# Kernel tuning notes

Measured on AMD Instinct MI355X. Metric: run time of the kernel, lower is better.

Reference implementation:

```python
import jax, jax.numpy as jnp
import numpy as np

N_NODES = 100000
N_FEAT = 512
HIDDEN = 64
N_CLASSES = 40
N_EDGES = 3200000
K = 10
ALPHA = 0.1


def setup_inputs() -> dict:
    key = jax.random.key(0)
    k1, k2, k3, k4 = jax.random.split(key, 4)
    x = jax.random.normal(k1, (N_NODES, N_FEAT), dtype=jnp.float32)
    # Glorot-ish scaled linear weights
    W1 = jax.random.normal(k2, (N_FEAT, HIDDEN), dtype=jnp.float32) / np.sqrt(N_FEAT)
    b1 = jnp.zeros((HIDDEN,), dtype=jnp.float32)
    W2 = jax.random.normal(k3, (HIDDEN, N_CLASSES), dtype=jnp.float32) / np.sqrt(HIDDEN)
    b2 = jnp.zeros((N_CLASSES,), dtype=jnp.float32)
    edge_index = jax.random.randint(k4, (2, N_EDGES), 0, N_NODES, dtype=jnp.int64)
    return {"x": x, "W1": W1, "b1": b1, "W2": W2, "b2": b2, "edge_index": edge_index}


def reference(x, W1, b1, W2, b2, edge_index):
    n = x.shape[0]
    # MLP (dropout is identity in eval mode)
    h = jnp.maximum(x @ W1 + b1, 0.0)
    h = h @ W2 + b2  # [N, C]

    # gcn_norm with self-loops: A_hat = D^{-1/2} (A + I) D^{-1/2}
    loops = jnp.arange(n, dtype=edge_index.dtype)
    row = jnp.concatenate([edge_index[0], loops])  # source (gather)
    col = jnp.concatenate([edge_index[1], loops])  # target (scatter)
    deg = jax.ops.segment_sum(jnp.ones(row.shape, dtype=h.dtype), col, num_segments=n)
    dinv = jnp.where(deg > 0, jax.lax.rsqrt(deg), 0.0)
    norm = dinv[row] * dinv[col]  # [E + N]

    h0 = h

    def step(z, _):
        msg = norm[:, None] * z[row]                      # gather + scale
        agg = jax.ops.segment_sum(msg, col, num_segments=n)  # scatter-add
        z = ALPHA * h0 + (1.0 - ALPHA) * agg
        return z, None

    z, _ = jax.lax.scan(step, h0, None, length=K)
    return jax.nn.log_softmax(z, axis=1)
```

## Files before the change

kernel.cpp:

```cpp
#include <hip/hip_runtime.h>
#include <hip/hip_bf16.h>
#include <hip/hip_fp16.h>

#define N_NODES   100000
#define N_FEAT    512
#define HIDDEN    64
#define N_CLASSES 40
#define KITER     10
#define ALPHA     0.1f
#define ZP        64
#define HPITCH    72

typedef __attribute__((ext_vector_type(8))) short bf16x8;
typedef __attribute__((ext_vector_type(4))) float f32x4;

__device__ __forceinline__ float bf2f(unsigned short u) {
    union { unsigned int i; float f; } c;
    c.i = ((unsigned int)u) << 16;
    return c.f;
}
__device__ __forceinline__ unsigned short f2bf(float f) {
    union { float f; unsigned int u; } c; c.f = f;
    unsigned int r = c.u + 0x7FFFu + ((c.u >> 16) & 1u);
    return (unsigned short)(r >> 16);
}

__global__ void zero_flags_kernel(int* __restrict__ flags) {
    if (threadIdx.x < 2) flags[threadIdx.x] = 0;
}

__global__ void detect_float_kernel(const unsigned short* __restrict__ w1raw,
                                    int* __restrict__ flags) {
    int i = blockIdx.x * blockDim.x + threadIdx.x;
    if (i < 32768) {
        unsigned short u = w1raw[i];
        if ((u & 0x7F80u) == 0x7F80u) atomicAdd(&flags[0], 1);
    }
}

__global__ void detect_edge_kernel(const int* __restrict__ ei, int* __restrict__ flags) {
    int i = blockIdx.x * blockDim.x + threadIdx.x;
    if (i < 2048) {
        if (ei[2 * i + 1] != 0) atomicAdd(&flags[1], 1);
    }
}

__device__ __forceinline__ int edge_row(const int* ei, int e, int E, int i64f) {
    return i64f ? ei[2 * e] : ei[e];
}
__device__ __forceinline__ int edge_col(const int* ei, int e, int E, int i64f) {
    return i64f ? ei[2 * E + 2 * e] : ei[E + e];
}

__global__ void pack_w1_kernel(const void* __restrict__ W1p, const int* __restrict__ flags,
                               unsigned short* __restrict__ pb) {
    int idx = blockIdx.x * 256 + threadIdx.x;
    int j    = idx & 7;
    int lane = (idx >> 3) & 63;
    int ktnt = idx >> 9;
    int kt = ktnt & 15, nt = ktnt >> 4;
    int k = kt * 32 + (lane >> 4) * 8 + j;
    int n = nt * 16 + (lane & 15);
    unsigned short v;
    if (flags[0] > 0) v = f2bf(((const float*)W1p)[k * HIDDEN + n]);
    else              v = ((const unsigned short*)W1p)[k * HIDDEN + n];
    pb[idx] = v;
}

__global__ void pack_w2_kernel(const void* __restrict__ W2p, const int* __restrict__ flags,
                               unsigned short* __restrict__ pb2) {
    int idx = blockIdx.x * 256 + threadIdx.x;
    if (idx >= 3072) return;
    int j    = idx & 7;
    int lane = (idx >> 3) & 63;
    int ktnt = idx >> 9;
    int kt = ktnt & 1, nt = ktnt >> 1;
    int k = kt * 32 + (lane >> 4) * 8 + j;
    int n = nt * 16 + (lane & 15);
    unsigned short v = 0;
    if (n < N_CLASSES) {
        if (flags[0] > 0) v = f2bf(((const float*)W2p)[k * N_CLASSES + n]);
        else              v = ((const unsigned short*)W2p)[k * N_CLASSES + n];
    }
    pb2[idx] = v;
}

__global__ __launch_bounds__(256) void mlp_kernel(
    const void* __restrict__ xp,
    const unsigned short* __restrict__ pb,
    const unsigned short* __restrict__ pb2,
    const void* __restrict__ b1p,
    const void* __restrict__ b2p,
    const int* __restrict__ flags,
    float* __restrict__ h0,
    __half* __restrict__ zh0)
{
    __shared__ unsigned short hsb[16 * HPITCH];
    const int t    = threadIdx.x;
    const int wave = t >> 6;
    const int lane = t & 63;
    const int quad = lane >> 4;
    const int ml   = lane & 15;
    const int base = blockIdx.x * 16;
    const int isf32 = flags[0] > 0;

    const bf16x8* pbv = (const bf16x8*)pb;

    f32x4 acc = {0.f, 0.f, 0.f, 0.f};
    if (!isf32) {
        const unsigned short* xrow = (const unsigned short*)xp
                                   + (size_t)(base + ml) * N_FEAT + quad * 8;
        #pragma unroll
        for (int kt = 0; kt < 16; ++kt) {
            bf16x8 a = *(const bf16x8*)(xrow + kt * 32);
            bf16x8 b = pbv[(wave * 16 + kt) * 64 + lane];
            acc = __builtin_amdgcn_mfma_f32_16x16x32_bf16(a, b, acc, 0, 0, 0);
        }
    } else {
        const float* xf = (const float*)xp + (size_t)(base + ml) * N_FEAT + quad * 8;
        #pragma unroll
        for (int kt = 0; kt < 16; ++kt) {
            float4 lo = *(const float4*)(xf + kt * 32);
            float4 hi = *(const float4*)(xf + kt * 32 + 4);
            bf16x8 a;
            a[0] = (short)f2bf(lo.x); a[1] = (short)f2bf(lo.y);
            a[2] = (short)f2bf(lo.z); a[3] = (short)f2bf(lo.w);
            a[4] = (short)f2bf(hi.x); a[5] = (short)f2bf(hi.y);
            a[6] = (short)f2bf(hi.z); a[7] = (short)f2bf(hi.w);
            bf16x8 b = pbv[(wave * 16 + kt) * 64 + lane];
            acc = __builtin_amdgcn_mfma_f32_16x16x32_bf16(a, b, acc, 0, 0, 0);
        }
    }

    float b1v = isf32 ? ((const float*)b1p)[wave * 16 + ml]
                      : bf2f(((const unsigned short*)b1p)[wave * 16 + ml]);
    #pragma unroll
    for (int r = 0; r < 4; ++r)
        hsb[(quad * 4 + r) * HPITCH + wave * 16 + ml] = f2bf(fmaxf(acc[r] + b1v, 0.0f));
    __syncthreads();

    if (wave < 3) {
        const bf16x8* pb2v = (const bf16x8*)pb2;
        f32x4 acc2 = {0.f, 0.f, 0.f, 0.f};
        #pragma unroll
        for (int kt = 0; kt < 2; ++kt) {
            bf16x8 a = *(const bf16x8*)(hsb + ml * HPITCH + kt * 32 + quad * 8);
            bf16x8 b = pb2v[(wave * 2 + kt) * 64 + lane];
            acc2 = __builtin_amdgcn_mfma_f32_16x16x32_bf16(a, b, acc2, 0, 0, 0);
        }
        int n = wave * 16 + ml;
        if (n < N_CLASSES) {
            float b2v = isf32 ? ((const float*)b2p)[n] : bf2f(((const unsigned short*)b2p)[n]);
            #pragma unroll
            for (int r = 0; r < 4; ++r) {
                int node = base + quad * 4 + r;
                float v = acc2[r] + b2v;
                h0[(size_t)node * N_CLASSES + n] = v;
                zh0[(size_t)node * ZP + n] = __float2half(v);
            }
        }
    }
}

__global__ void zero_cnt_kernel(int* __restrict__ cnt) {
    int i = blockIdx.x * blockDim.x + threadIdx.x;
    if (i < N_NODES) cnt[i] = 0;
}

__global__ void count_kernel(const int* __restrict__ ei, const int* __restrict__ flags,
                             int* __restrict__ cnt, int E) {
    int e = blockIdx.x * blockDim.x + threadIdx.x;
    int i64f = flags[1] == 0;
    if (e < E) atomicAdd(&cnt[edge_col(ei, e, E, i64f)], 1);
}

__global__ void dinv_kernel(const int* __restrict__ cnt, float* __restrict__ dinv) {
    int i = blockIdx.x * blockDim.x + threadIdx.x;
    if (i < N_NODES) dinv[i] = rsqrtf((float)cnt[i] + 1.0f);
}

__global__ __launch_bounds__(1024) void scan_kernel(
    const int* __restrict__ cnt, int* __restrict__ rptr, int* __restrict__ wpos, int E)
{
    __shared__ int wsum[16];
    __shared__ int carry_s, tiletot_s;
    const int t = threadIdx.x, wave = t >> 6, lane = t & 63;
    if (t == 0) carry_s = 0;
    __syncthreads();
    for (int base = 0; base < N_NODES; base += 4096) {
        int i0 = base + t * 4;
        int v0 = (i0 + 0 < N_NODES) ? cnt[i0 + 0] : 0;
        int v1 = (i0 + 1 < N_NODES) ? cnt[i0 + 1] : 0;
        int v2 = (i0 + 2 < N_NODES) ? cnt[i0 + 2] : 0;
        int v3 = (i0 + 3 < N_NODES) ? cnt[i0 + 3] : 0;
        int tl = v0 + v1 + v2 + v3;
        int sc = tl;
        #pragma unroll
        for (int off = 1; off < 64; off <<= 1) {
            int u = __shfl_up(sc, off, 64);
            if (lane >= off) sc += u;
        }
        if (lane == 63) wsum[wave] = sc;
        int wexcl = sc - tl;
        __syncthreads();
        if (wave == 0) {
            int wv = (lane < 16) ? wsum[lane] : 0;
            int ws = wv;
            #pragma unroll
            for (int off = 1; off < 16; off <<= 1) {
                int u = __shfl_up(ws, off, 64);
                if (lane >= off) ws += u;
            }
            if (lane < 16) wsum[lane] = ws - wv;
            if (lane == 15) tiletot_s = ws;
        }
        __syncthreads();
        int P  = carry_s + wsum[wave] + wexcl;
        int e0 = P, e1 = P + v0, e2 = e1 + v1, e3 = e2 + v2;
        if (i0 + 0 < N_NODES) { rptr[i0 + 0] = e0; wpos[i0 + 0] = e0; }
        if (i0 + 1 < N_NODES) { rptr[i0 + 1] = e1; wpos[i0 + 1] = e1; }
        if (i0 + 2 < N_NODES) { rptr[i0 + 2] = e2; wpos[i0 + 2] = e2; }
        if (i0 + 3 < N_NODES) { rptr[i0 + 3] = e3; wpos[i0 + 3] = e3; }
        __syncthreads();
        if (t == 0) carry_s += tiletot_s;
        __syncthreads();
    }
    if (t == 0) rptr[N_NODES] = E;
}

__global__ void fill_kernel(const int* __restrict__ ei, const int* __restrict__ flags,
                            const float* __restrict__ dinv, int* __restrict__ wpos,
                            int2* __restrict__ srn, int E)
{
    int e = blockIdx.x * blockDim.x + threadIdx.x;
    int i64f = flags[1] == 0;
    if (e < E) {
        int r = edge_row(ei, e, E, i64f);
        int c = edge_col(ei, e, E, i64f);
        int pos = atomicAdd(&wpos[c], 1);
        srn[pos] = make_int2(r, __float_as_int(dinv[r] * dinv[c]));
    }
}

__global__ __launch_bounds__(256) void prop_kernel(
    const __half* __restrict__ zh, const float* __restrict__ h0,
    const float* __restrict__ dinv, const int* __restrict__ rptr,
    const int2* __restrict__ srn, __half* __restrict__ zout, int E)
{
    const int wave = threadIdx.x >> 6;
    const int lane = threadIdx.x & 63;
    const int g    = lane >> 4;
    const int l    = lane & 15;
    const int node = blockIdx.x * 16 + wave * 4 + g;
    const int c0   = l * 4;

    const int beg = rptr[node];
    const int end = rptr[node + 1];
    int nch = (end - beg + 15) >> 4;
    int m1    = max(nch, __shfl_xor(nch, 16, 64));
    int maxch = max(m1,  __shfl_xor(m1, 32, 64));

    float di = dinv[node];
    uint2 zzs = *(const uint2*)(zh + ((size_t)node << 6) + c0);
    float h00 = 0.f, h01 = 0.f, h02 = 0.f, h03 = 0.f;
    if (c0 < N_CLASSES) {
        const float* hp = h0 + (size_t)node * N_CLASSES + c0;
        h00 = hp[0]; h01 = hp[1]; h02 = hp[2]; h03 = hp[3];
    }

    float a0 = 0.f, a1 = 0.f, a2 = 0.f, a3 = 0.f;
    float b0 = 0.f, b1 = 0.f, b2 = 0.f, b3 = 0.f;

    for (int ch = 0; ch < maxch; ++ch) {
        int idx  = beg + ch * 16 + l;
        bool v   = idx < end;
        int cidx = v ? idx : beg;
        cidx = min(cidx, E - 1);
        int2 ew  = srn[cidx];
        int   sw = ew.x;
        float nw = v ? __int_as_float(ew.y) : 0.0f;

        #pragma unroll
        for (int i = 0; i < 16; i += 2) {
            int   s0 = __shfl(sw, (g << 4) + i,     64);
            float n0 = __shfl(nw, (g << 4) + i,     64);
            int   s1 = __shfl(sw, (g << 4) + i + 1, 64);
            float n1 = __shfl(nw, (g << 4) + i + 1, 64);
            uint2 z0 = *(const uint2*)(zh + ((size_t)s0 << 6) + c0);
            uint2 z1 = *(const uint2*)(zh + ((size_t)s1 << 6) + c0);
            const __half2* p0 = (const __half2*)&z0;
            const __half2* p1 = (const __half2*)&z1;
            float2 f00 = __half22float2(p0[0]);
            float2 f01 = __half22float2(p0[1]);
            float2 f10 = __half22float2(p1[0]);
            float2 f11 = __half22float2(p1[1]);
            a0 = fmaf(n0, f00.x, a0); a1 = fmaf(n0, f00.y, a1);
            a2 = fmaf(n0, f01.x, a2); a3 = fmaf(n0, f01.y, a3);
            b0 = fmaf(n1, f10.x, b0); b1 = fmaf(n1, f10.y, b1);
            b2 = fmaf(n1, f11.x, b2); b3 = fmaf(n1, f11.y, b3);
        }
    }

    if (c0 < N_CLASSES) {
        const __half2* ps = (const __half2*)&zzs;
        float2 s01 = __half22float2(ps[0]);
        float2 s23 = __half22float2(ps[1]);
        float dd = di * di;
        float o0 = ALPHA * h00 + (1.0f - ALPHA) * (a0 + b0 + dd * s01.x);
        float o1 = ALPHA * h01 + (1.0f - ALPHA) * (a1 + b1 + dd * s01.y);
        float o2 = ALPHA * h02 + (1.0f - ALPHA) * (a2 + b2 + dd * s23.x);
        float o3 = ALPHA * h03 + (1.0f - ALPHA) * (a3 + b3 + dd * s23.y);
        __half2 q01 = __floats2half2_rn(o0, o1);
        __half2 q23 = __floats2half2_rn(o2, o3);
        uint2 st;
        st.x = *(unsigned int*)&q01;
        st.y = *(unsigned int*)&q23;
        *(uint2*)(zout + ((size_t)node << 6) + c0) = st;
    }
}

__global__ __launch_bounds__(256) void lsm_kernel(
    const __half* __restrict__ zh, const int* __restrict__ flags, void* __restrict__ outp)
{
    const int wave = threadIdx.x >> 6;
    const int lane = threadIdx.x & 63;
    const int node = blockIdx.x * 4 + wave;
    const int isf32 = flags[0] > 0;

    float v = (lane < N_CLASSES) ? __half2float(zh[(size_t)node * ZP + lane]) : -1e30f;
    float m = v;
    #pragma unroll
    for (int o = 32; o; o >>= 1) m = fmaxf(m, __shfl_xor(m, o, 64));
    float e = (lane < N_CLASSES) ? expf(v - m) : 0.0f;
    float s = e;
    #pragma unroll
    for (int o = 32; o; o >>= 1) s += __shfl_xor(s, o, 64);
    float ls = logf(s);
    if (lane < N_CLASSES) {
        float r = v - m - ls;
        size_t idx = (size_t)node * N_CLASSES + lane;
        if (isf32) ((float*)outp)[idx] = r;
        else       ((__hip_bfloat16*)outp)[idx] = __float2bfloat16(r);
    }
}

extern "C" void kernel_launch(void* const* d_in, const int* in_sizes, int n_in,
                              void* d_out, int out_size, void* d_ws, size_t ws_size,
                              hipStream_t stream)
{
    const void* x  = d_in[0];
    const void* W1 = d_in[1];
    const void* b1 = d_in[2];
    const void* W2 = d_in[3];
    const void* b2 = d_in[4];
    const int* ei = (const int*)d_in[5];
    const int E = in_sizes[5] / 2;

    char* ws = (char*)d_ws;
    size_t off = 0;
    auto carve = [&](size_t bytes) -> void* {
        void* p = ws + off;
        off = (off + bytes + 255) & ~(size_t)255;
        return p;
    };
    float*  h0    = (float*) carve((size_t)N_NODES * N_CLASSES * 4);
    __half* zhA   = (__half*)carve((size_t)N_NODES * ZP * 2);
    __half* zhB   = (__half*)carve((size_t)N_NODES * ZP * 2);
    int*    cnt   = (int*)   carve((size_t)N_NODES * 4);
    float*  dinv  = (float*) carve((size_t)N_NODES * 4);
    int*    rptr  = (int*)   carve((size_t)(N_NODES + 1) * 4);
    int*    wpos  = (int*)   carve((size_t)N_NODES * 4);
    int2*   srn   = (int2*)  carve((size_t)E * 8);
    unsigned short* pb  = (unsigned short*)carve(32768 * 2);
    unsigned short* pb2 = (unsigned short*)carve(3072 * 2);
    int*    flags = (int*)   carve(2 * sizeof(int));
    (void)ws_size; (void)n_in; (void)out_size;

    const int nodeBlocks = N_NODES / 4;
    const int mlpBlocks  = N_NODES / 16;
    const int propBlocks = N_NODES / 16;
    const int nThreads1  = (N_NODES + 255) / 256;
    const int eBlocks    = (E + 255) / 256;

    zero_flags_kernel<<<1, 64, 0, stream>>>(flags);
    detect_float_kernel<<<128, 256, 0, stream>>>((const unsigned short*)W1, flags);
    detect_edge_kernel<<<8, 256, 0, stream>>>(ei, flags);
    pack_w1_kernel<<<128, 256, 0, stream>>>(W1, flags, pb);
    pack_w2_kernel<<<12, 256, 0, stream>>>(W2, flags, pb2);

    mlp_kernel<<<mlpBlocks, 256, 0, stream>>>(x, pb, pb2, b1, b2, flags, h0, zhA);

    zero_cnt_kernel<<<nThreads1, 256, 0, stream>>>(cnt);
    count_kernel<<<eBlocks, 256, 0, stream>>>(ei, flags, cnt, E);
    dinv_kernel<<<nThreads1, 256, 0, stream>>>(cnt, dinv);
    scan_kernel<<<1, 1024, 0, stream>>>(cnt, rptr, wpos, E);
    fill_kernel<<<eBlocks, 256, 0, stream>>>(ei, flags, dinv, wpos, srn, E);

    const __half* zin = zhA;
    __half* zout = zhB;
    const __half* zlast = zhA;
    for (int it = 0; it < KITER; ++it) {
        prop_kernel<<<propBlocks, 256, 0, stream>>>(zin, h0, dinv, rptr, srn, zout, E);
        zlast = zout;
        zin = zout;
        zout = (zout == zhB) ? zhA : zhB;
    }

    lsm_kernel<<<nodeBlocks, 256, 0, stream>>>(zlast, flags, d_out);
}
```

Before: 1.274 ms.

## Store dinv-prescaled features and drop per-edge weights; window CSR fill by destination

Propagation state is now stored as dinv-scaled features, so each edge needs only a source index and the per-edge normalization weight disappears. This halves the CSR edge payload and removes a multiply per gathered element. A dummy zero row at index N_NODES replaces per-lane validity masking. The CSR fill kernel now makes eight windowed passes over destination ranges to localize its atomics and scattered writes, at the cost of re-reading edges. Scaling by dinv before fp16 storage, then dividing back in log-softmax, changes rounding behaviour.

New measurement: 1.300 ms. 2.1% more time.

```diff
diff --git a/kernel.cpp b/kernel.cpp
--- a/kernel.cpp
+++ b/kernel.cpp
@@ -10,6 +10,10 @@
 #define ALPHA     0.1f
 #define ZP        64
 #define HPITCH    72
+#define NPASS     8
+#define WIN       (N_NODES / NPASS)
+#define FILLB     2048
+#define SLOTS     7
 
 typedef __attribute__((ext_vector_type(8))) short bf16x8;
 typedef __attribute__((ext_vector_type(4))) float f32x4;
@@ -92,6 +96,7 @@
     const void* __restrict__ b1p,
     const void* __restrict__ b2p,
     const int* __restrict__ flags,
+    const float* __restrict__ dinv,
     float* __restrict__ h0,
     __half* __restrict__ zh0)
 {
@@ -156,7 +161,7 @@
                 int node = base + quad * 4 + r;
                 float v = acc2[r] + b2v;
                 h0[(size_t)node * N_CLASSES + n] = v;
-                zh0[(size_t)node * ZP + n] = __float2half(v);
+                zh0[(size_t)node * ZP + n] = __float2half(v * dinv[node]);
             }
         }
     }
@@ -177,6 +182,12 @@
 __global__ void dinv_kernel(const int* __restrict__ cnt, float* __restrict__ dinv) {
     int i = blockIdx.x * blockDim.x + threadIdx.x;
     if (i < N_NODES) dinv[i] = rsqrtf((float)cnt[i] + 1.0f);
+}
+
+__global__ void zero_pad_kernel(__half* __restrict__ a, __half* __restrict__ b) {
+    int t = threadIdx.x;
+    if (t < ZP)            a[(size_t)N_NODES * ZP + t]        = __float2half(0.0f);
+    else if (t < 2 * ZP)   b[(size_t)N_NODES * ZP + (t - ZP)] = __float2half(0.0f);
 }
 
 __global__ __launch_bounds__(1024) void scan_kernel(
@@ -228,24 +239,44 @@
     if (t == 0) rptr[N_NODES] = E;
 }
 
-__global__ void fill_kernel(const int* __restrict__ ei, const int* __restrict__ flags,
-                            const float* __restrict__ dinv, int* __restrict__ wpos,
-                            int2* __restrict__ srn, int E)
-{
-    int e = blockIdx.x * blockDim.x + threadIdx.x;
-    int i64f = flags[1] == 0;
-    if (e < E) {
-        int r = edge_row(ei, e, E, i64f);
-        int c = edge_col(ei, e, E, i64f);
-        int pos = atomicAdd(&wpos[c], 1);
-        srn[pos] = make_int2(r, __float_as_int(dinv[r] * dinv[c]));
+__global__ __launch_bounds__(256) void fill8_kernel(
+    const int* __restrict__ ei, const int* __restrict__ flags,
+    int* __restrict__ wpos, int* __restrict__ srcidx, int E)
+{
+    const int i64f = flags[1] == 0;
+    const int t0 = blockIdx.x * 256 + threadIdx.x;
+    const int stride = FILLB * 256;
+    int rk[SLOTS], ck[SLOTS];
+    #pragma unroll
+    for (int k = 0; k < SLOTS; ++k) {
+        int e = t0 + k * stride;
+        rk[k] = -1; ck[k] = -1;
+        if (e < E) { rk[k] = edge_row(ei, e, E, i64f); ck[k] = edge_col(ei, e, E, i64f); }
+    }
+    #pragma unroll
+    for (int p = 0; p < NPASS; ++p) {
+        int lo = p * WIN;
+        #pragma unroll
+        for (int k = 0; k < SLOTS; ++k) {
+            if ((unsigned)(ck[k] - lo) < (unsigned)WIN) {
+                int pos = atomicAdd(&wpos[ck[k]], 1);
+                srcidx[pos] = rk[k];
+            }
+        }
+        for (int e = t0 + SLOTS * stride; e < E; e += stride) {
+            int c = edge_col(ei, e, E, i64f);
+            if ((unsigned)(c - lo) < (unsigned)WIN) {
+                int pos = atomicAdd(&wpos[c], 1);
+                srcidx[pos] = edge_row(ei, e, E, i64f);
+            }
+        }
     }
 }
 
 __global__ __launch_bounds__(256) void prop_kernel(
     const __half* __restrict__ zh, const float* __restrict__ h0,
     const float* __restrict__ dinv, const int* __restrict__ rptr,
-    const int2* __restrict__ srn, __half* __restrict__ zout, int E)
+    const int* __restrict__ srcidx, __half* __restrict__ zout)
 {
     const int wave = threadIdx.x >> 6;
     const int lane = threadIdx.x & 63;
@@ -261,7 +292,7 @@
     int maxch = max(m1,  __shfl_xor(m1, 32, 64));
 
     float di = dinv[node];
-    uint2 zzs = *(const uint2*)(zh + ((size_t)node << 6) + c0);
+    uint2 yself = *(const uint2*)(zh + ((size_t)node << 6) + c0);
     float h00 = 0.f, h01 = 0.f, h02 = 0.f, h03 = 0.f;
     if (c0 < N_CLASSES) {
         const float* hp = h0 + (size_t)node * N_CLASSES + c0;
@@ -272,20 +303,13 @@
     float b0 = 0.f, b1 = 0.f, b2 = 0.f, b3 = 0.f;
 
     for (int ch = 0; ch < maxch; ++ch) {
-        int idx  = beg + ch * 16 + l;
-        bool v   = idx < end;
-        int cidx = v ? idx : beg;
-        cidx = min(cidx, E - 1);
-        int2 ew  = srn[cidx];
-        int   sw = ew.x;
-        float nw = v ? __int_as_float(ew.y) : 0.0f;
+        int idx = beg + ch * 16 + l;
+        int sw  = (idx < end) ? srcidx[idx] : N_NODES;
 
         #pragma unroll
         for (int i = 0; i < 16; i += 2) {
-            int   s0 = __shfl(sw, (g << 4) + i,     64);
-            float n0 = __shfl(nw, (g << 4) + i,     64);
-            int   s1 = __shfl(sw, (g << 4) + i + 1, 64);
-            float n1 = __shfl(nw, (g << 4) + i + 1, 64);
+            int s0 = __shfl(sw, (g << 4) + i,     64);
+            int s1 = __shfl(sw, (g << 4) + i + 1, 64);
             uint2 z0 = *(const uint2*)(zh + ((size_t)s0 << 6) + c0);
             uint2 z1 = *(const uint2*)(zh + ((size_t)s1 << 6) + c0);
             const __half2* p0 = (const __half2*)&z0;
@@ -294,24 +318,22 @@
             float2 f01 = __half22float2(p0[1]);
             float2 f10 = __half22float2(p1[0]);
             float2 f11 = __half22float2(p1[1]);
-            a0 = fmaf(n0, f00.x, a0); a1 = fmaf(n0, f00.y, a1);
-            a2 = fmaf(n0, f01.x, a2); a3 = fmaf(n0, f01.y, a3);
-            b0 = fmaf(n1, f10.x, b0); b1 = fmaf(n1, f10.y, b1);
-            b2 = fmaf(n1, f11.x, b2); b3 = fmaf(n1, f11.y, b3);
+            a0 += f00.x; a1 += f00.y; a2 += f01.x; a3 += f01.y;
+            b0 += f10.x; b1 += f10.y; b2 += f11.x; b3 += f11.y;
         }
     }
 
     if (c0 < N_CLASSES) {
-        const __half2* ps = (const __half2*)&zzs;
+        const __half2* ps = (const __half2*)&yself;
         float2 s01 = __half22float2(ps[0]);
         float2 s23 = __half22float2(ps[1]);
-        float dd = di * di;
-        float o0 = ALPHA * h00 + (1.0f - ALPHA) * (a0 + b0 + dd * s01.x);
-        float o1 = ALPHA * h01 + (1.0f - ALPHA) * (a1 + b1 + dd * s01.y);
-        float o2 = ALPHA * h02 + (1.0f - ALPHA) * (a2 + b2 + dd * s23.x);
-        float o3 = ALPHA * h03 + (1.0f - ALPHA) * (a3 + b3 + dd * s23.y);
-        __half2 q01 = __floats2half2_rn(o0, o1);
-        __half2 q23 = __floats2half2_rn(o2, o3);
+        float kk = (1.0f - ALPHA) * di;
+        float o0 = ALPHA * h00 + kk * (a0 + b0 + s01.x);
+        float o1 = ALPHA * h01 + kk * (a1 + b1 + s01.y);
+        float o2 = ALPHA * h02 + kk * (a2 + b2 + s23.x);
+        float o3 = ALPHA * h03 + kk * (a3 + b3 + s23.y);
+        __half2 q01 = __floats2half2_rn(di * o0, di * o1);
+        __half2 q23 = __floats2half2_rn(di * o2, di * o3);
         uint2 st;
         st.x = *(unsigned int*)&q01;
         st.y = *(unsigned int*)&q23;
@@ -320,14 +342,17 @@
 }
 
 __global__ __launch_bounds__(256) void lsm_kernel(
-    const __half* __restrict__ zh, const int* __restrict__ flags, void* __restrict__ outp)
+    const __half* __restrict__ zh, const float* __restrict__ dinv,
+    const int* __restrict__ flags, void* __restrict__ outp)
 {
     const int wave = threadIdx.x >> 6;
     const int lane = threadIdx.x & 63;
     const int node = blockIdx.x * 4 + wave;
     const int isf32 = flags[0] > 0;
 
-    float v = (lane < N_CLASSES) ? __half2float(zh[(size_t)node * ZP + lane]) : -1e30f;
+    float di = dinv[node];
+    float v = (lane < N_CLASSES)
+            ? __half2float(zh[(size_t)node * ZP + lane]) / di : -1e30f;
     float m = v;
     #pragma unroll
     for (int o = 32; o; o >>= 1) m = fmaxf(m, __shfl_xor(m, o, 64));
@@ -364,13 +389,13 @@
         return p;
     };
     float*  h0    = (float*) carve((size_t)N_NODES * N_CLASSES * 4);
-    __half* zhA   = (__half*)carve((size_t)N_NODES * ZP * 2);
-    __half* zhB   = (__half*)carve((size_t)N_NODES * ZP * 2);
+    __half* zhA   = (__half*)carve((size_t)(N_NODES + 1) * ZP * 2);
+    __half* zhB   = (__half*)carve((size_t)(N_NODES + 1) * ZP * 2);
     int*    cnt   = (int*)   carve((size_t)N_NODES * 4);
     float*  dinv  = (float*) carve((size_t)N_NODES * 4);
     int*    rptr  = (int*)   carve((size_t)(N_NODES + 1) * 4);
     int*    wpos  = (int*)   carve((size_t)N_NODES * 4);
-    int2*   srn   = (int2*)  carve((size_t)E * 8);
+    int*    srcidx= (int*)   carve((size_t)E * 4);
     unsigned short* pb  = (unsigned short*)carve(32768 * 2);
     unsigned short* pb2 = (unsigned short*)carve(3072 * 2);
     int*    flags = (int*)   carve(2 * sizeof(int));
@@ -388,23 +413,24 @@
     pack_w1_kernel<<<128, 256, 0, stream>>>(W1, flags, pb);
     pack_w2_kernel<<<12, 256, 0, stream>>>(W2, flags, pb2);
 
-    mlp_kernel<<<mlpBlocks, 256, 0, stream>>>(x, pb, pb2, b1, b2, flags, h0, zhA);
-
     zero_cnt_kernel<<<nThreads1, 256, 0, stream>>>(cnt);
     count_kernel<<<eBlocks, 256, 0, stream>>>(ei, flags, cnt, E);
     dinv_kernel<<<nThreads1, 256, 0, stream>>>(cnt, dinv);
     scan_kernel<<<1, 1024, 0, stream>>>(cnt, rptr, wpos, E);
-    fill_kernel<<<eBlocks, 256, 0, stream>>>(ei, flags, dinv, wpos, srn, E);
+    fill8_kernel<<<FILLB, 256, 0, stream>>>(ei, flags, wpos, srcidx, E);
+    zero_pad_kernel<<<1, 128, 0, stream>>>(zhA, zhB);
+
+    mlp_kernel<<<mlpBlocks, 256, 0, stream>>>(x, pb, pb2, b1, b2, flags, dinv, h0, zhA);
 
     const __half* zin = zhA;
     __half* zout = zhB;
     const __half* zlast = zhA;
     for (int it = 0; it < KITER; ++it) {
-        prop_kernel<<<propBlocks, 256, 0, stream>>>(zin, h0, dinv, rptr, srn, zout, E);
+        prop_kernel<<<propBlocks, 256, 0, stream>>>(zin, h0, dinv, rptr, srcidx, zout);
         zlast = zout;
         zin = zout;
         zout = (zout == zhB) ? zhA : zhB;
     }
 
-    lsm_kernel<<<nodeBlocks, 256, 0, stream>>>(zlast, flags, d_out);
-}
+    lsm_kernel<<<nodeBlocks, 256, 0, stream>>>(zlast, dinv, flags, d_out);
+}
```
